# Kernel tuning notes

Hardware: AMD Instinct MI355X
Metric: run time of the kernel (lower is better)

## Reference

```python
import jax, jax.numpy as jnp
import numpy as np

N_NODES = 100000
N_EDGES = 1600000
D_IN = 128
D_HID = 128
N_CLASS = 10
N_GRAPHS = 512
BN_EPS = 1e-5


def setup_inputs() -> dict:
    key = jax.random.key(0)
    ks = jax.random.split(key, 12)
    x = jax.random.normal(ks[0], (N_NODES, D_IN), dtype=jnp.float32)
    edge_index = jax.random.randint(ks[1], (2, N_EDGES), 0, N_NODES, dtype=jnp.int32)
    idx = jnp.sort(jax.random.randint(ks[2], (N_NODES,), 0, N_GRAPHS, dtype=jnp.int32))
    s = 1.0 / np.sqrt(D_HID)
    W1 = jax.random.uniform(ks[3], (D_IN, D_HID), minval=-s, maxval=s, dtype=jnp.float32)
    b1 = jnp.zeros((D_HID,), jnp.float32)
    W2 = jax.random.uniform(ks[4], (D_HID, D_HID), minval=-s, maxval=s, dtype=jnp.float32)
    b2 = jnp.zeros((D_HID,), jnp.float32)
    W3 = jax.random.uniform(ks[5], (D_HID, D_HID), minval=-s, maxval=s, dtype=jnp.float32)
    b3 = jnp.zeros((D_HID,), jnp.float32)
    W4 = jax.random.uniform(ks[6], (D_HID, N_CLASS), minval=-s, maxval=s, dtype=jnp.float32)
    b4 = jnp.zeros((N_CLASS,), jnp.float32)
    gamma = jnp.ones((D_HID,), jnp.float32)
    beta = jnp.zeros((D_HID,), jnp.float32)
    return {"x": x, "edge_index": edge_index, "idx": idx,
            "W1": W1, "b1": b1, "W2": W2, "b2": b2,
            "W3": W3, "b3": b3, "W4": W4, "b4": b4,
            "gamma": gamma, "beta": beta}


def _agg(h, src, dst):
    # (adj + I) @ h : sum of neighbor features plus self-loop
    return jax.ops.segment_sum(h[src], dst, num_segments=N_NODES) + h


def reference(x, edge_index, idx, W1, b1, W2, b2, W3, b3, W4, b4, gamma, beta):
    src, dst = edge_index[0], edge_index[1]
    z1 = jax.nn.relu(_agg(x, src, dst) @ W1 + b1)          # [N, H] (dropout = identity, eval)
    h = _agg(z1, src, dst) @ W2 + b2                        # [N, H]
    pooled = jax.ops.segment_sum(h, idx, num_segments=N_GRAPHS)  # [G, H] scatter-add readout
    # BatchNorm1d over graph (batch) dimension, training-mode batch stats
    mean = jnp.mean(pooled, axis=0)
    var = jnp.var(pooled, axis=0)
    out = (pooled - mean) * jax.lax.rsqrt(var + BN_EPS) * gamma + beta
    zg = jax.nn.relu(out @ W3 + b3)
    logits = zg @ W4 + b4                                   # [G, C]
    return jax.nn.log_softmax(logits, axis=1)
```

## Files before the change

### kernel.cpp

```cpp
#include <hip/hip_runtime.h>
#include <hip/hip_fp16.h>
#include <math.h>

#define NN 100000
#define NE 1600000
#define DH 128
#define NG 512
#define NC 10
#define NSEG 8
#define SEGN 12500
#define CHE 4096
#define NCH 391
#define MAXDEG 48
#define WPITCH 136

#define NB_HIST (NCH * NSEG)
#define NB_CNT  98

typedef __attribute__((ext_vector_type(8))) _Float16 f16x8;
typedef __attribute__((ext_vector_type(4))) float f32x4;


__global__ __launch_bounds__(256) void k_hist(const int* __restrict__ dst,
                                              const int* __restrict__ src,
                                              int* __restrict__ counts,
                                              int* __restrict__ csr,
                                              const int* __restrict__ gidx,
                                              int* __restrict__ cnt) {
    int b = blockIdx.x;
    int t = threadIdx.x;
    if (b < NB_HIST) {
        int seg = b & 7;
        int chunk = b >> 3;
        int lo = seg * SEGN, hi = lo + SEGN;
        int e0 = chunk * CHE;
        int e1 = e0 + CHE < NE ? e0 + CHE : NE;
        for (int e = e0 + t * 4; e < e1; e += 1024) {
            int4 d4 = *(const int4*)(dst + e);
            bool i0 = d4.x >= lo && d4.x < hi;
            bool i1 = d4.y >= lo && d4.y < hi;
            bool i2 = d4.z >= lo && d4.z < hi;
            bool i3 = d4.w >= lo && d4.w < hi;
            int4 s4 = {0, 0, 0, 0};
            if (i0 | i1 | i2 | i3) s4 = *(const int4*)(src + e);
            if (i0) {
                int p = atomicAdd(&counts[d4.x], 1);
                if (p < MAXDEG) csr[d4.x * MAXDEG + p] = s4.x;
            }
            if (i1) {
                int p = atomicAdd(&counts[d4.y], 1);
                if (p < MAXDEG) csr[d4.y * MAXDEG + p] = s4.y;
            }
            if (i2) {
                int p = atomicAdd(&counts[d4.z], 1);
                if (p < MAXDEG) csr[d4.z * MAXDEG + p] = s4.z;
            }
            if (i3) {
                int p = atomicAdd(&counts[d4.w], 1);
                if (p < MAXDEG) csr[d4.w * MAXDEG + p] = s4.w;
            }
        }
    } else {
        int cb = b - NB_HIST;
        int n0 = cb * 1024 + t * 4;
        if (n0 >= NN) return;
        int g = gidx[n0];
        int run = 1;
        for (int j = 1; j < 4; ++j) {
            int n = n0 + j;
            if (n < NN) {
                int gg = gidx[n];
                if (gg == g) {
                    run++;
                } else {
                    atomicAdd(&cnt[g], run);
                    g = gg;
                    run = 1;
                }
            }
        }
        atomicAdd(&cnt[g], run);
    }
}


__global__ __launch_bounds__(256, 3) void k_mm_mfma(
    const float* __restrict__ A, const float* __restrict__ W,
    __half* __restrict__ out) {
    __shared__ _Float16 sWT[DH * WPITCH];
    __shared__ __align__(16) _Float16 sOut[4][16][DH];
    int t = threadIdx.x;
    int wv = t >> 6;
    int lane = t & 63;
    for (int i = t; i < DH * DH; i += 256) {
        int k = i >> 7, n = i & 127;
        sWT[n * WPITCH + k] = (_Float16)W[i];
    }
    __syncthreads();

    int m = lane & 15;
    int quad = lane >> 4;
    int node0 = blockIdx.x * 64 + wv * 16;
    int nodeA = node0 + m;
    if (nodeA >= NN) nodeA = NN - 1;
    const float* arow = A + (size_t)nodeA * DH;

    f16x8 afrag[4];
#pragma unroll
    for (int kt = 0; kt < 4; ++kt) {
        int k0 = kt * 32 + quad * 8;
        float4 u0 = *(const float4*)(arow + k0);
        float4 u1 = *(const float4*)(arow + k0 + 4);
        afrag[kt][0] = (_Float16)u0.x; afrag[kt][1] = (_Float16)u0.y;
        afrag[kt][2] = (_Float16)u0.z; afrag[kt][3] = (_Float16)u0.w;
        afrag[kt][4] = (_Float16)u1.x; afrag[kt][5] = (_Float16)u1.y;
        afrag[kt][6] = (_Float16)u1.z; afrag[kt][7] = (_Float16)u1.w;
    }

#pragma unroll
    for (int ct = 0; ct < 8; ++ct) {
        f32x4 acc = {0.f, 0.f, 0.f, 0.f};
        int n = ct * 16 + m;
#pragma unroll
        for (int kt = 0; kt < 4; ++kt) {
            int k0 = kt * 32 + quad * 8;
            f16x8 bfrag = *(const f16x8*)&sWT[n * WPITCH + k0];
            acc = __builtin_amdgcn_mfma_f32_16x16x32_f16(afrag[kt], bfrag, acc, 0, 0, 0);
        }
#pragma unroll
        for (int r = 0; r < 4; ++r)
            sOut[wv][quad * 4 + r][ct * 16 + m] = (_Float16)acc[r];
    }
    __syncthreads();

    const uint4* so = (const uint4*)&sOut[wv][0][0];
    for (int i = lane; i < 256; i += 64) {
        int row = i >> 4;
        int node = node0 + row;
        if (node < NN) ((uint4*)out)[(size_t)node * 16 + (i & 15)] = so[i];
    }
}


__device__ __forceinline__ void acc8(float* a, const uint4& v, float m) {
    float2 f;
    f = __half22float2(*(const __half2*)&v.x); a[0] = fmaf(m, f.x, a[0]); a[1] = fmaf(m, f.y, a[1]);
    f = __half22float2(*(const __half2*)&v.y); a[2] = fmaf(m, f.x, a[2]); a[3] = fmaf(m, f.y, a[3]);
    f = __half22float2(*(const __half2*)&v.z); a[4] = fmaf(m, f.x, a[4]); a[5] = fmaf(m, f.y, a[5]);
    f = __half22float2(*(const __half2*)&v.w); a[6] = fmaf(m, f.x, a[6]); a[7] = fmaf(m, f.y, a[7]);
}


__global__ __launch_bounds__(256, 4) void k_agg_h(
    const __half* __restrict__ in, const int* __restrict__ counts,
    const int* __restrict__ csr, const float* __restrict__ bias,
    __half* __restrict__ outA) {
    int t = threadIdx.x;
    int lane = t & 15;
    int node = blockIdx.x * 16 + (t >> 4);
    const uint4* in4 = (const uint4*)in;
    float a[8];
#pragma unroll
    for (int j = 0; j < 8; ++j) a[j] = 0.f;
    uint4 sv = in4[(size_t)node * 16 + lane];
    acc8(a, sv, 1.f);
    int e0 = node * MAXDEG;
    int deg = counts[node];
    deg = deg < MAXDEG ? deg : MAXDEG;
    int e1 = e0 + deg;
    int elast = e1 - 1;
    for (int e = e0; e < e1; e += 8) {
        int idx[8];
        float m[8];
#pragma unroll
        for (int i = 0; i < 8; ++i) {
            int ei = e + i;
            int ec = ei < elast ? ei : elast;
            idx[i] = csr[ec];
            m[i] = (ei < e1) ? 1.f : 0.f;
        }
        uint4 v[8];
#pragma unroll
        for (int i = 0; i < 8; ++i) v[i] = in4[(size_t)idx[i] * 16 + lane];
#pragma unroll
        for (int i = 0; i < 8; ++i) acc8(a, v[i], m[i]);
    }
    float4 b0 = ((const float4*)bias)[lane * 2];
    float4 b1v = ((const float4*)bias)[lane * 2 + 1];
    a[0] = fmaxf(a[0] + b0.x, 0.f);  a[1] = fmaxf(a[1] + b0.y, 0.f);
    a[2] = fmaxf(a[2] + b0.z, 0.f);  a[3] = fmaxf(a[3] + b0.w, 0.f);
    a[4] = fmaxf(a[4] + b1v.x, 0.f); a[5] = fmaxf(a[5] + b1v.y, 0.f);
    a[6] = fmaxf(a[6] + b1v.z, 0.f); a[7] = fmaxf(a[7] + b1v.w, 0.f);
    uint4 o;
    *(__half2*)&o.x = __floats2half2_rn(a[0], a[1]);
    *(__half2*)&o.y = __floats2half2_rn(a[2], a[3]);
    *(__half2*)&o.z = __floats2half2_rn(a[4], a[5]);
    *(__half2*)&o.w = __floats2half2_rn(a[6], a[7]);
    ((uint4*)outA)[(size_t)node * 16 + lane] = o;
}


__global__ __launch_bounds__(256, 4) void k_agg_pool_h(
    const __half* __restrict__ in, const int* __restrict__ counts,
    const int* __restrict__ csr, const int* __restrict__ gidx,
    float* __restrict__ pp8) {
    __shared__ __align__(16) float sA[16][DH];
    int t = threadIdx.x;
    int lane = t & 15;
    int p = t >> 4;
    int node0 = blockIdx.x * 16;
    int node = node0 + p;
    const uint4* in4 = (const uint4*)in;
    float a[8];
#pragma unroll
    for (int j = 0; j < 8; ++j) a[j] = 0.f;
    uint4 sv = in4[(size_t)node * 16 + lane];
    acc8(a, sv, 1.f);
    int e0 = node * MAXDEG;
    int deg = counts[node];
    deg = deg < MAXDEG ? deg : MAXDEG;
    int e1 = e0 + deg;
    int elast = e1 - 1;
    for (int e = e0; e < e1; e += 8) {
        int idx[8];
        float m[8];
#pragma unroll
        for (int i = 0; i < 8; ++i) {
            int ei = e + i;
            int ec = ei < elast ? ei : elast;
            idx[i] = csr[ec];
            m[i] = (ei < e1) ? 1.f : 0.f;
        }
        uint4 v[8];
#pragma unroll
        for (int i = 0; i < 8; ++i) v[i] = in4[(size_t)idx[i] * 16 + lane];
#pragma unroll
        for (int i = 0; i < 8; ++i) acc8(a, v[i], m[i]);
    }
    float4* row = (float4*)&sA[p][lane * 8];
    row[0] = make_float4(a[0], a[1], a[2], a[3]);
    row[1] = make_float4(a[4], a[5], a[6], a[7]);
    __syncthreads();
    if (t < DH) {
        float* pp = pp8 + (size_t)(blockIdx.x & 7) * NG * DH;
        int gprev = gidx[node0];
        float run = 0.f;
        for (int q = 0; q < 16; ++q) {
            int g = gidx[node0 + q];
            if (g != gprev) {
                atomicAdd(&pp[gprev * DH + t], run);
                run = 0.f;
                gprev = g;
            }
            run += sA[q][t];
        }
        atomicAdd(&pp[gprev * DH + t], run);
    }
}


__device__ __forceinline__ void fma4(float4& acc, float s, const float4& wv) {
    acc.x = fmaf(s, wv.x, acc.x);
    acc.y = fmaf(s, wv.y, acc.y);
    acc.z = fmaf(s, wv.z, acc.z);
    acc.w = fmaf(s, wv.w, acc.w);
}


__global__ __launch_bounds__(256, 2) void k_pool_mm(
    const float* __restrict__ pp8, const float* __restrict__ W,
    const float* __restrict__ bias, const int* __restrict__ cnt,
    float* __restrict__ pooled) {
    __shared__ __align__(16) float sW[DH * DH];
    __shared__ __align__(16) float sA[32 * DH];
    int t = threadIdx.x;
    int g0 = blockIdx.x * 32;
    {
        const float4* W4g = (const float4*)W;
        float4* sW4 = (float4*)sW;
        for (int i = t; i < DH * DH / 4; i += 256) sW4[i] = W4g[i];
        const float4* P4 = (const float4*)pp8;
        float4* sA4 = (float4*)sA;
        for (int i = t; i < 32 * DH / 4; i += 256) {
            float4 s;
            s.x = 0.f; s.y = 0.f; s.z = 0.f; s.w = 0.f;
#pragma unroll
            for (int c = 0; c < NSEG; ++c) {
                float4 v = P4[(size_t)c * NG * DH / 4 + (size_t)g0 * DH / 4 + i];
                s.x += v.x; s.y += v.y; s.z += v.z; s.w += v.w;
            }
            sA4[i] = s;
        }
    }
    __syncthreads();

    int c4 = t & 31;
    int n0 = (t >> 5) * 4;
    const float4* sA4 = (const float4*)sA;
    const float4* sW4 = (const float4*)sW;
    float4 acc0, acc1, acc2, acc3;
    acc0.x = acc0.y = acc0.z = acc0.w = 0.f;
    acc1 = acc0; acc2 = acc0; acc3 = acc0;

#pragma unroll 2
    for (int kc = 0; kc < DH / 4; ++kc) {
        float4 a0 = sA4[(n0 + 0) * 32 + kc];
        float4 a1 = sA4[(n0 + 1) * 32 + kc];
        float4 a2 = sA4[(n0 + 2) * 32 + kc];
        float4 a3 = sA4[(n0 + 3) * 32 + kc];
        float4 w0 = sW4[(4 * kc + 0) * 32 + c4];
        float4 w1 = sW4[(4 * kc + 1) * 32 + c4];
        float4 w2 = sW4[(4 * kc + 2) * 32 + c4];
        float4 w3 = sW4[(4 * kc + 3) * 32 + c4];
        fma4(acc0, a0.x, w0); fma4(acc0, a0.y, w1); fma4(acc0, a0.z, w2); fma4(acc0, a0.w, w3);
        fma4(acc1, a1.x, w0); fma4(acc1, a1.y, w1); fma4(acc1, a1.z, w2); fma4(acc1, a1.w, w3);
        fma4(acc2, a2.x, w0); fma4(acc2, a2.y, w1); fma4(acc2, a2.z, w2); fma4(acc2, a2.w, w3);
        fma4(acc3, a3.x, w0); fma4(acc3, a3.y, w1); fma4(acc3, a3.z, w2); fma4(acc3, a3.w, w3);
    }

    float4 b2v = ((const float4*)bias)[c4];
    float c0 = (float)cnt[g0 + n0 + 0];
    float c1 = (float)cnt[g0 + n0 + 1];
    float c2 = (float)cnt[g0 + n0 + 2];
    float c3 = (float)cnt[g0 + n0 + 3];
    fma4(acc0, c0, b2v);
    fma4(acc1, c1, b2v);
    fma4(acc2, c2, b2v);
    fma4(acc3, c3, b2v);

    float4* out4 = (float4*)pooled;
    out4[(size_t)(g0 + n0 + 0) * 32 + c4] = acc0;
    out4[(size_t)(g0 + n0 + 1) * 32 + c4] = acc1;
    out4[(size_t)(g0 + n0 + 2) * 32 + c4] = acc2;
    out4[(size_t)(g0 + n0 + 3) * 32 + c4] = acc3;
}


__global__ void k_bnstats(const float* __restrict__ pooled, float* __restrict__ mean,
                          float* __restrict__ rstd) {
    int c = blockIdx.x;
    int l = threadIdx.x;
    float s = 0.f, s2 = 0.f;
    for (int g = l; g < NG; g += 64) {
        float v = pooled[g * DH + c];
        s += v;
        s2 += v * v;
    }
#pragma unroll
    for (int off = 32; off > 0; off >>= 1) {
        s += __shfl_down(s, off, 64);
        s2 += __shfl_down(s2, off, 64);
    }
    if (l == 0) {
        float m = s * (1.f / NG);
        float var = s2 * (1.f / NG) - m * m;
        mean[c] = m;
        rstd[c] = rsqrtf(var + 1e-5f);
    }
}


__global__ __launch_bounds__(128) void k_tail(
    const float* __restrict__ pooled, const float* __restrict__ mean,
    const float* __restrict__ rstd, const float* __restrict__ gamma,
    const float* __restrict__ beta, const float* __restrict__ W3,
    const float* __restrict__ b3, const float* __restrict__ W4,
    const float* __restrict__ b4, float* __restrict__ out) {
    __shared__ __align__(16) float sW[DH * DH];
    __shared__ float sg[DH];
    __shared__ float sz[DH];
    __shared__ float slog[NC];
    __shared__ float slse;
    int g = blockIdx.x, t = threadIdx.x;
    {
        const float4* W34 = (const float4*)W3;
        float4* sW4 = (float4*)sW;
        for (int i = t; i < DH * DH / 4; i += 128) sW4[i] = W34[i];
    }
    float v = pooled[g * DH + t];
    v = (v - mean[t]) * rstd[t] * gamma[t] + beta[t];
    sg[t] = v;
    __syncthreads();
    float acc = b3[t];
#pragma unroll 4
    for (int k = 0; k < DH; ++k) acc = fmaf(sg[k], sW[k * DH + t], acc);
    sz[t] = fmaxf(acc, 0.f);
    __syncthreads();
    if (t < NC) {
        float a = b4[t];
        for (int k = 0; k < DH; ++k) a = fmaf(sz[k], W4[k * NC + t], a);
        slog[t] = a;
    }
    __syncthreads();
    if (t == 0) {
        float mx = slog[0];
        for (int j = 1; j < NC; ++j) mx = fmaxf(mx, slog[j]);
        float se = 0.f;
        for (int j = 0; j < NC; ++j) se += expf(slog[j] - mx);
        slse = mx + logf(se);
    }
    __syncthreads();
    if (t < NC) out[g * NC + t] = slog[t] - slse;
}


extern "C" void kernel_launch(void* const* d_in, const int* in_sizes, int n_in,
                              void* d_out, int out_size, void* d_ws, size_t ws_size,
                              hipStream_t stream) {
    const float* x = (const float*)d_in[0];
    const int* ei = (const int*)d_in[1];
    const int* src = ei;
    const int* dst = ei + NE;
    const int* gidx = (const int*)d_in[2];
    const float* W1 = (const float*)d_in[3];
    const float* b1 = (const float*)d_in[4];
    const float* W2 = (const float*)d_in[5];
    const float* b2 = (const float*)d_in[6];
    const float* W3 = (const float*)d_in[7];
    const float* b3 = (const float*)d_in[8];
    const float* W4 = (const float*)d_in[9];
    const float* b4 = (const float*)d_in[10];
    const float* gamma = (const float*)d_in[11];
    const float* beta = (const float*)d_in[12];
    float* out = (float*)d_out;

    char* w = (char*)d_ws;
    auto take = [&](size_t bytes) {
        char* p = w;
        w += (bytes + 255) & ~size_t(255);
        return p;
    };
    int* counts = (int*)take((size_t)NN * 4);
    int* cnt = (int*)take((size_t)NG * 4);
    float* pp8 = (float*)take((size_t)NSEG * NG * DH * 4);
    size_t zero_bytes = (size_t)((char*)(pp8 + (size_t)NSEG * NG * DH) - (char*)counts);
    int* csr = (int*)take((size_t)NN * MAXDEG * 4);
    __half* y = (__half*)take((size_t)NN * DH * 2);
    __half* z1 = (__half*)take((size_t)NN * DH * 2);
    float* pooled = (float*)take((size_t)NG * DH * 4);
    float* meanb = (float*)take(DH * 4);
    float* rstdb = (float*)take(DH * 4);

    hipMemsetAsync(counts, 0, zero_bytes, stream);

    k_hist<<<NB_HIST + NB_CNT, 256, 0, stream>>>(dst, src, counts, csr, gidx, cnt);

    k_mm_mfma<<<(NN + 63) / 64, 256, 0, stream>>>(x, W1, y);
    k_agg_h<<<NN / 16, 256, 0, stream>>>(y, counts, csr, b1, z1);

    k_agg_pool_h<<<NN / 16, 256, 0, stream>>>(z1, counts, csr, gidx, pp8);
    k_pool_mm<<<NG / 32, 256, 0, stream>>>(pp8, W2, b2, cnt, pooled);

    k_bnstats<<<DH, 64, 0, stream>>>(pooled, meanb, rstdb);
    k_tail<<<NG, 128, 0, stream>>>(pooled, meanb, rstdb, gamma, beta, W3, b3, W4, b4, out);
}
```

Measured before the change: 364.0 us.

## Fuse BN stats into pool matmul, use nontemporal loads, enlarge histogram chunks

Removes the separate batch-norm statistics kernel. k_pool_mm now reduces per-channel sum and sum of squares for its 32 graphs through shared memory and adds them atomically into global buffers, and k_tail derives mean and rstd from those. Edge, CSR and count reads in the histogram and aggregation kernels become nontemporal loads, and the histogram chunk size doubles so half as many blocks are launched. The fused stats use float atomics, so the summation order is nondeterministic, and fewer histogram blocks may reduce parallelism.

```diff
diff --git a/kernel.cpp b/kernel.cpp
--- a/kernel.cpp
+++ b/kernel.cpp
@@ -9,8 +9,8 @@
 #define NC 10
 #define NSEG 8
 #define SEGN 12500
-#define CHE 4096
-#define NCH 391
+#define CHE 8192
+#define NCH 196
 #define MAXDEG 48
 #define WPITCH 136
 
@@ -19,6 +19,7 @@
 
 typedef __attribute__((ext_vector_type(8))) _Float16 f16x8;
 typedef __attribute__((ext_vector_type(4))) float f32x4;
+typedef __attribute__((ext_vector_type(4))) int v4i;
 
 
 __global__ __launch_bounds__(256) void k_hist(const int* __restrict__ dst,
@@ -36,13 +37,14 @@
         int e0 = chunk * CHE;
         int e1 = e0 + CHE < NE ? e0 + CHE : NE;
         for (int e = e0 + t * 4; e < e1; e += 1024) {
-            int4 d4 = *(const int4*)(dst + e);
+            v4i d4 = __builtin_nontemporal_load((const v4i*)(dst + e));
             bool i0 = d4.x >= lo && d4.x < hi;
             bool i1 = d4.y >= lo && d4.y < hi;
             bool i2 = d4.z >= lo && d4.z < hi;
             bool i3 = d4.w >= lo && d4.w < hi;
-            int4 s4 = {0, 0, 0, 0};
-            if (i0 | i1 | i2 | i3) s4 = *(const int4*)(src + e);
+            v4i s4 = {0, 0, 0, 0};
+            if (i0 | i1 | i2 | i3)
+                s4 = __builtin_nontemporal_load((const v4i*)(src + e));
             if (i0) {
                 int p = atomicAdd(&counts[d4.x], 1);
                 if (p < MAXDEG) csr[d4.x * MAXDEG + p] = s4.x;
@@ -165,7 +167,7 @@
     uint4 sv = in4[(size_t)node * 16 + lane];
     acc8(a, sv, 1.f);
     int e0 = node * MAXDEG;
-    int deg = counts[node];
+    int deg = __builtin_nontemporal_load(counts + node);
     deg = deg < MAXDEG ? deg : MAXDEG;
     int e1 = e0 + deg;
     int elast = e1 - 1;
@@ -176,7 +178,7 @@
         for (int i = 0; i < 8; ++i) {
             int ei = e + i;
             int ec = ei < elast ? ei : elast;
-            idx[i] = csr[ec];
+            idx[i] = __builtin_nontemporal_load(csr + ec);
             m[i] = (ei < e1) ? 1.f : 0.f;
         }
         uint4 v[8];
@@ -217,7 +219,7 @@
     uint4 sv = in4[(size_t)node * 16 + lane];
     acc8(a, sv, 1.f);
     int e0 = node * MAXDEG;
-    int deg = counts[node];
+    int deg = __builtin_nontemporal_load(counts + node);
     deg = deg < MAXDEG ? deg : MAXDEG;
     int e1 = e0 + deg;
     int elast = e1 - 1;
@@ -228,7 +230,7 @@
         for (int i = 0; i < 8; ++i) {
             int ei = e + i;
             int ec = ei < elast ? ei : elast;
-            idx[i] = csr[ec];
+            idx[i] = __builtin_nontemporal_load(csr + ec);
             m[i] = (ei < e1) ? 1.f : 0.f;
         }
         uint4 v[8];
@@ -270,7 +272,8 @@
 __global__ __launch_bounds__(256, 2) void k_pool_mm(
     const float* __restrict__ pp8, const float* __restrict__ W,
     const float* __restrict__ bias, const int* __restrict__ cnt,
-    float* __restrict__ pooled) {
+    float* __restrict__ pooled, float* __restrict__ gsum,
+    float* __restrict__ gsum2) {
     __shared__ __align__(16) float sW[DH * DH];
     __shared__ __align__(16) float sA[32 * DH];
     int t = threadIdx.x;
@@ -333,36 +336,30 @@
     out4[(size_t)(g0 + n0 + 1) * 32 + c4] = acc1;
     out4[(size_t)(g0 + n0 + 2) * 32 + c4] = acc2;
     out4[(size_t)(g0 + n0 + 3) * 32 + c4] = acc3;
-}
-
-
-__global__ void k_bnstats(const float* __restrict__ pooled, float* __restrict__ mean,
-                          float* __restrict__ rstd) {
-    int c = blockIdx.x;
-    int l = threadIdx.x;
-    float s = 0.f, s2 = 0.f;
-    for (int g = l; g < NG; g += 64) {
-        float v = pooled[g * DH + c];
-        s += v;
-        s2 += v * v;
-    }
-#pragma unroll
-    for (int off = 32; off > 0; off >>= 1) {
-        s += __shfl_down(s, off, 64);
-        s2 += __shfl_down(s2, off, 64);
-    }
-    if (l == 0) {
-        float m = s * (1.f / NG);
-        float var = s2 * (1.f / NG) - m * m;
-        mean[c] = m;
-        rstd[c] = rsqrtf(var + 1e-5f);
+
+    __syncthreads();
+    float4* sA4w = (float4*)sA;
+    sA4w[(n0 + 0) * 32 + c4] = acc0;
+    sA4w[(n0 + 1) * 32 + c4] = acc1;
+    sA4w[(n0 + 2) * 32 + c4] = acc2;
+    sA4w[(n0 + 3) * 32 + c4] = acc3;
+    __syncthreads();
+    if (t < DH) {
+        float s = 0.f, s2 = 0.f;
+        for (int g = 0; g < 32; ++g) {
+            float v = sA[g * DH + t];
+            s += v;
+            s2 += v * v;
+        }
+        atomicAdd(&gsum[t], s);
+        atomicAdd(&gsum2[t], s2);
     }
 }
 
 
 __global__ __launch_bounds__(128) void k_tail(
-    const float* __restrict__ pooled, const float* __restrict__ mean,
-    const float* __restrict__ rstd, const float* __restrict__ gamma,
+    const float* __restrict__ pooled, const float* __restrict__ gsum,
+    const float* __restrict__ gsum2, const float* __restrict__ gamma,
     const float* __restrict__ beta, const float* __restrict__ W3,
     const float* __restrict__ b3, const float* __restrict__ W4,
     const float* __restrict__ b4, float* __restrict__ out) {
@@ -377,8 +374,11 @@
         float4* sW4 = (float4*)sW;
         for (int i = t; i < DH * DH / 4; i += 128) sW4[i] = W34[i];
     }
+    float mean = gsum[t] * (1.f / NG);
+    float var = gsum2[t] * (1.f / NG) - mean * mean;
+    float rstd = rsqrtf(var + 1e-5f);
     float v = pooled[g * DH + t];
-    v = (v - mean[t]) * rstd[t] * gamma[t] + beta[t];
+    v = (v - mean) * rstd * gamma[t] + beta[t];
     sg[t] = v;
     __syncthreads();
     float acc = b3[t];
@@ -433,13 +433,13 @@
     int* counts = (int*)take((size_t)NN * 4);
     int* cnt = (int*)take((size_t)NG * 4);
     float* pp8 = (float*)take((size_t)NSEG * NG * DH * 4);
-    size_t zero_bytes = (size_t)((char*)(pp8 + (size_t)NSEG * NG * DH) - (char*)counts);
+    float* gsum = (float*)take(DH * 4);
+    float* gsum2 = (float*)take(DH * 4);
+    size_t zero_bytes = (size_t)((char*)(gsum2 + DH) - (char*)counts);
     int* csr = (int*)take((size_t)NN * MAXDEG * 4);
     __half* y = (__half*)take((size_t)NN * DH * 2);
     __half* z1 = (__half*)take((size_t)NN * DH * 2);
     float* pooled = (float*)take((size_t)NG * DH * 4);
-    float* meanb = (float*)take(DH * 4);
-    float* rstdb = (float*)take(DH * 4);
 
     hipMemsetAsync(counts, 0, zero_bytes, stream);
 
@@ -449,8 +449,7 @@
     k_agg_h<<<NN / 16, 256, 0, stream>>>(y, counts, csr, b1, z1);
 
     k_agg_pool_h<<<NN / 16, 256, 0, stream>>>(z1, counts, csr, gidx, pp8);
-    k_pool_mm<<<NG / 32, 256, 0, stream>>>(pp8, W2, b2, cnt, pooled);
-
-    k_bnstats<<<DH, 64, 0, stream>>>(pooled, meanb, rstdb);
-    k_tail<<<NG, 128, 0, stream>>>(pooled, meanb, rstdb, gamma, beta, W3, b3, W4, b4, out);
-}
+    k_pool_mm<<<NG / 32, 256, 0, stream>>>(pp8, W2, b2, cnt, pooled, gsum, gsum2);
+
+    k_tail<<<NG, 128, 0, stream>>>(pooled, gsum, gsum2, gamma, beta, W3, b3, W4, b4, out);
+}
```

New measurement: 374.0 us. +2.7%, slower.
